# Kernel optimization log

Measured on AMD Instinct MI355X. Metric: run time of the kernel, lower is better.

Reference implementation:

```python
import jax, jax.numpy as jnp
import numpy as np

BLOCK = 32      # MX block size (elements sharing one scale)
EMAX = 8        # e4m3 max biased-unbias exponent (max normal = 448 = 2^8 * 1.75)
EMIN = -6       # e4m3 min normal exponent (values below handled as subnormal grid)
MAN_BITS = 3    # e4m3 mantissa bits
MAXVAL = 448.0  # e4m3 max representable magnitude


def _fp8_e4m3(x):
    """Round x to the nearest FP8 E4M3 representable value (saturating)."""
    absx = jnp.abs(x)
    # exponent of each element, clipped to normal range; EMIN clip gives the subnormal grid
    e = jnp.clip(jnp.floor(jnp.log2(jnp.where(absx > 0, absx, 1.0))), EMIN, EMAX)
    quantum = jnp.exp2(e - MAN_BITS)          # spacing of representable values at this exponent
    q = jnp.round(absx / quantum) * quantum   # round-to-nearest on that grid
    return jnp.sign(x) * jnp.minimum(q, MAXVAL)


def mx_fake_quant(x):
    """MX (microscaling) fake quantization: per-32-element power-of-two shared
    scale from block amax, elements stored as FP8 E4M3, then dequantized."""
    shape = x.shape
    xb = x.reshape(-1, BLOCK)                                   # [n_blocks, 32]
    amax = jnp.max(jnp.abs(xb), axis=-1, keepdims=True)         # [n_blocks, 1]
    # shared exponent: floor(log2(amax)) - emax_elem  (E8M0 power-of-two scale)
    shared_exp = jnp.floor(jnp.log2(jnp.where(amax > 0, amax, 1.0))) - EMAX
    scale = jnp.exp2(shared_exp)
    xq = _fp8_e4m3(xb / scale) * scale
    return xq.reshape(shape)


@jax.custom_vjp
def mx_ste(x):
    return mx_fake_quant(x)


def _mx_fwd(x):
    return mx_fake_quant(x), None


def _mx_bwd(_, g):
    return (g,)  # straight-through estimator


mx_ste.defvjp(_mx_fwd, _mx_bwd)


def setup_inputs() -> dict:
    key = jax.random.key(0)
    k1, k2 = jax.random.split(key)
    d_in, d_out = 256, 256
    x = jax.random.normal(k1, (16, 8192, d_in), dtype=jnp.float32)
    # lecun_normal init: std = 1/sqrt(fan_in)
    kernel = jax.random.normal(k2, (d_in, d_out), dtype=jnp.float32) * (1.0 / np.sqrt(d_in))
    bias = jnp.zeros((d_out,), dtype=jnp.float32)
    return {"x": x, "kernel": kernel, "bias": bias}


def reference(x, kernel, bias):
    xq = mx_ste(x)        # quantize_input=True
    kq = mx_ste(kernel)   # weight quantizer
    return jnp.dot(xq, kq) + bias
```

## Files before the change

### kernel.cpp

```cpp
#include <hip/hip_runtime.h>
#include <hip/hip_bf16.h>

typedef unsigned short u16;
typedef unsigned int u32;
typedef __attribute__((ext_vector_type(8))) short bf16x8;
typedef __attribute__((ext_vector_type(4))) float f32x4;
typedef __attribute__((ext_vector_type(2))) float f32x2;
typedef __attribute__((ext_vector_type(4))) unsigned short u16x4;

__device__ __forceinline__ void block_scale(float amax, float& scale, float& inv_scale) {
    int be = (int)(__float_as_uint(amax) >> 23);
    be = be < 8 ? 8 : be;
    scale     = __uint_as_float((unsigned)(be - 8) << 23);
    inv_scale = __uint_as_float((unsigned)(262 - be) << 23);
}

#if __has_builtin(__builtin_amdgcn_cvt_pk_fp8_f32) && __has_builtin(__builtin_amdgcn_cvt_pk_f32_fp8)
#define HAS_HW_FP8 1
#else
#define HAS_HW_FP8 0
#endif

#if !HAS_HW_FP8
__device__ __forceinline__ float mx_e4m3(float x, float inv_scale, float scale) {
    float v  = x * inv_scale;
    float av = fabsf(v);
    int e = (int)(__float_as_uint(av) >> 23) - 127;
    e = e < -6 ? -6 : (e > 8 ? 8 : e);
    float qs = __uint_as_float((unsigned)(130 - e) << 23);
    float qm = __uint_as_float((unsigned)(124 + e) << 23);
    float q  = fminf(rintf(av * qs) * qm, 448.0f);
    return copysignf(q, v) * scale;
}
#endif

__device__ __forceinline__ u16x4 quant4(float4 v, float inv, float sc) {
    u16x4 r;
#if HAS_HW_FP8
    float a = fminf(fmaxf(v.x * inv, -448.f), 448.f);
    float b = fminf(fmaxf(v.y * inv, -448.f), 448.f);
    float c = fminf(fmaxf(v.z * inv, -448.f), 448.f);
    float d = fminf(fmaxf(v.w * inv, -448.f), 448.f);
    int p = __builtin_amdgcn_cvt_pk_fp8_f32(a, b, 0, false);
    p     = __builtin_amdgcn_cvt_pk_fp8_f32(c, d, p, true);
    f32x2 lo = __builtin_amdgcn_cvt_pk_f32_fp8(p, false);
    f32x2 hi = __builtin_amdgcn_cvt_pk_f32_fp8(p, true);
    r.x = (u16)(__float_as_uint(lo[0] * sc) >> 16);
    r.y = (u16)(__float_as_uint(lo[1] * sc) >> 16);
    r.z = (u16)(__float_as_uint(hi[0] * sc) >> 16);
    r.w = (u16)(__float_as_uint(hi[1] * sc) >> 16);
#else
    r.x = (u16)(__float_as_uint(mx_e4m3(v.x, inv, sc)) >> 16);
    r.y = (u16)(__float_as_uint(mx_e4m3(v.y, inv, sc)) >> 16);
    r.z = (u16)(__float_as_uint(mx_e4m3(v.z, inv, sc)) >> 16);
    r.w = (u16)(__float_as_uint(mx_e4m3(v.w, inv, sc)) >> 16);
#endif
    return r;
}

__global__ void wq_kernel(const float* __restrict__ W, u16* __restrict__ Bq) {
    const int t  = blockIdx.x * blockDim.x + threadIdx.x;
    const int f  = t * 4;
    const int k  = f >> 8;
    const int n0 = f & 255;
    const float4 v = *(const float4*)(W + f);
    float am = fmaxf(fmaxf(fabsf(v.x), fabsf(v.y)), fmaxf(fabsf(v.z), fabsf(v.w)));
    am = fmaxf(am, __shfl_xor(am, 1));
    am = fmaxf(am, __shfl_xor(am, 2));
    am = fmaxf(am, __shfl_xor(am, 4));
    float sc, inv; block_scale(am, sc, inv);
    u16x4 q = quant4(v, inv, sc);
    Bq[(size_t)(n0 + 0) * 256 + k] = q.x;
    Bq[(size_t)(n0 + 1) * 256 + k] = q.y;
    Bq[(size_t)(n0 + 2) * 256 + k] = q.z;
    Bq[(size_t)(n0 + 3) * 256 + k] = q.w;
}

__global__ void __launch_bounds__(256, 4)
mx_gemm(const float* __restrict__ X, const u16* __restrict__ Bq,
        const float* __restrict__ bias, float* __restrict__ out)
{
    __shared__ u16 A[64 * 256];
    const int tid = threadIdx.x;
    const int w   = tid >> 6;
    const int l   = tid & 63;
    const size_t row0 = (size_t)blockIdx.x * 64;

    {
        const int kc = l * 4;
        float4 xv[16];
        #pragma unroll
        for (int it = 0; it < 16; ++it)
            xv[it] = *(const float4*)(X + (row0 + w * 16 + it) * 256 + kc);
        #pragma unroll
        for (int it = 0; it < 16; ++it) {
            const int r = w * 16 + it;
            float4 v = xv[it];
            float am = fmaxf(fmaxf(fabsf(v.x), fabsf(v.y)), fmaxf(fabsf(v.z), fabsf(v.w)));
            am = fmaxf(am, __shfl_xor(am, 1));
            am = fmaxf(am, __shfl_xor(am, 2));
            am = fmaxf(am, __shfl_xor(am, 4));
            float sc, inv; block_scale(am, sc, inv);
            u16x4 q = quant4(v, inv, sc);
            char* dst = (char*)A + (((u32)(r * 512 + l * 8)) ^ ((u32)(r & 7) << 4));
            *(u16x4*)dst = q;
        }
    }
    __syncthreads();

    const int lr = l & 15;
    const int lg = l >> 4;
    f32x4 acc[4][4] = {};
    const u16* bb = Bq + (size_t)(w * 64 + lr) * 256 + lg * 8;

    bf16x8 bcur[4], bnxt[4];
    #pragma unroll
    for (int ct = 0; ct < 4; ++ct)
        bcur[ct] = *(const bf16x8*)(bb + (size_t)ct * 16 * 256);

    #pragma unroll
    for (int ks = 0; ks < 8; ++ks) {
        bf16x8 af[4];
        #pragma unroll
        for (int rt = 0; rt < 4; ++rt) {
            const int row = rt * 16 + lr;
            const u32 off = ((u32)(row * 512 + ks * 64 + lg * 16)) ^ ((u32)(lr & 7) << 4);
            af[rt] = *(const bf16x8*)((const char*)A + off);
        }
        if (ks < 7) {
            #pragma unroll
            for (int ct = 0; ct < 4; ++ct)
                bnxt[ct] = *(const bf16x8*)(bb + (size_t)ct * 16 * 256 + (ks + 1) * 32);
        }
        #pragma unroll
        for (int rt = 0; rt < 4; ++rt)
            #pragma unroll
            for (int ct = 0; ct < 4; ++ct)
                acc[rt][ct] = __builtin_amdgcn_mfma_f32_16x16x32_bf16(
                    bcur[ct], af[rt], acc[rt][ct], 0, 0, 0);
        if (ks < 7) {
            #pragma unroll
            for (int ct = 0; ct < 4; ++ct) bcur[ct] = bnxt[ct];
        }
    }

    #pragma unroll
    for (int ct = 0; ct < 4; ++ct) {
        const float4 bv = *(const float4*)(bias + w * 64 + ct * 16 + lg * 4);
        #pragma unroll
        for (int rt = 0; rt < 4; ++rt) {
            f32x4 o = acc[rt][ct];
            o[0] += bv.x; o[1] += bv.y; o[2] += bv.z; o[3] += bv.w;
            *(f32x4*)(out + (row0 + rt * 16 + lr) * 256 + w * 64 + ct * 16 + lg * 4) = o;
        }
    }
}

extern "C" void kernel_launch(void* const* d_in, const int* in_sizes, int n_in,
                              void* d_out, int out_size, void* d_ws, size_t ws_size,
                              hipStream_t stream) {
    const float* x    = (const float*)d_in[0];
    const float* wk   = (const float*)d_in[1];
    const float* bias = (const float*)d_in[2];
    float* out = (float*)d_out;
    u16* Bq    = (u16*)d_ws;
    const int M = in_sizes[0] / 256;
    wq_kernel<<<64, 256, 0, stream>>>(wk, Bq);
    mx_gemm<<<M / 64, 256, 0, stream>>>(x, Bq, bias, out);
}
```

Before: 70.01 us.

## Load activations directly into MFMA register fragments, dropping the LDS staging

Each wavefront now owns 16 rows and all 256 output columns. It loads X straight into the MFMA A-fragment layout, quantizes in registers using a cross-lane amax shuffle over lanes 16 and 32, and skips the shared-memory tile and __syncthreads. The cost removed is the LDS write/read round trip and the block barrier. In exchange every wave streams the full 256x256 quantized weight matrix from global memory/L2, so B traffic per row rises 4x. The new layout also has uncoalesced strided X loads, and register pressure rises with launch_bounds min-blocks removed.

```diff
diff --git a/kernel.cpp b/kernel.cpp
--- a/kernel.cpp
+++ b/kernel.cpp
@@ -76,83 +76,63 @@
     Bq[(size_t)(n0 + 3) * 256 + k] = q.w;
 }
 
-__global__ void __launch_bounds__(256, 4)
+__global__ void __launch_bounds__(256)
 mx_gemm(const float* __restrict__ X, const u16* __restrict__ Bq,
         const float* __restrict__ bias, float* __restrict__ out)
 {
-    __shared__ u16 A[64 * 256];
     const int tid = threadIdx.x;
-    const int w   = tid >> 6;
     const int l   = tid & 63;
-    const size_t row0 = (size_t)blockIdx.x * 64;
+    const int lr  = l & 15;
+    const int lg  = l >> 4;
+    const size_t wv = (size_t)blockIdx.x * 4 + (tid >> 6);
+    const size_t r0 = wv * 16;
 
-    {
-        const int kc = l * 4;
-        float4 xv[16];
-        #pragma unroll
-        for (int it = 0; it < 16; ++it)
-            xv[it] = *(const float4*)(X + (row0 + w * 16 + it) * 256 + kc);
-        #pragma unroll
-        for (int it = 0; it < 16; ++it) {
-            const int r = w * 16 + it;
-            float4 v = xv[it];
-            float am = fmaxf(fmaxf(fabsf(v.x), fabsf(v.y)), fmaxf(fabsf(v.z), fabsf(v.w)));
-            am = fmaxf(am, __shfl_xor(am, 1));
-            am = fmaxf(am, __shfl_xor(am, 2));
-            am = fmaxf(am, __shfl_xor(am, 4));
-            float sc, inv; block_scale(am, sc, inv);
-            u16x4 q = quant4(v, inv, sc);
-            char* dst = (char*)A + (((u32)(r * 512 + l * 8)) ^ ((u32)(r & 7) << 4));
-            *(u16x4*)dst = q;
-        }
-    }
-    __syncthreads();
-
-    const int lr = l & 15;
-    const int lg = l >> 4;
-    f32x4 acc[4][4] = {};
-    const u16* bb = Bq + (size_t)(w * 64 + lr) * 256 + lg * 8;
-
-    bf16x8 bcur[4], bnxt[4];
-    #pragma unroll
-    for (int ct = 0; ct < 4; ++ct)
-        bcur[ct] = *(const bf16x8*)(bb + (size_t)ct * 16 * 256);
-
+    const float* xp = X + (r0 + lr) * 256 + lg * 8;
+    float4 xv[16];
     #pragma unroll
     for (int ks = 0; ks < 8; ++ks) {
-        bf16x8 af[4];
+        xv[2 * ks]     = *(const float4*)(xp + ks * 32);
+        xv[2 * ks + 1] = *(const float4*)(xp + ks * 32 + 4);
+    }
+
+    bf16x8 abf[8];
+    #pragma unroll
+    for (int ks = 0; ks < 8; ++ks) {
+        const float4 v0 = xv[2 * ks], v1 = xv[2 * ks + 1];
+        float am = fmaxf(fmaxf(fabsf(v0.x), fabsf(v0.y)), fmaxf(fabsf(v0.z), fabsf(v0.w)));
+        am = fmaxf(am, fmaxf(fmaxf(fabsf(v1.x), fabsf(v1.y)), fmaxf(fabsf(v1.z), fabsf(v1.w))));
+        am = fmaxf(am, __shfl_xor(am, 16));
+        am = fmaxf(am, __shfl_xor(am, 32));
+        float sc, inv; block_scale(am, sc, inv);
+        const u16x4 q0 = quant4(v0, inv, sc);
+        const u16x4 q1 = quant4(v1, inv, sc);
+        bf16x8 a;
+        a[0] = (short)q0.x; a[1] = (short)q0.y; a[2] = (short)q0.z; a[3] = (short)q0.w;
+        a[4] = (short)q1.x; a[5] = (short)q1.y; a[6] = (short)q1.z; a[7] = (short)q1.w;
+        abf[ks] = a;
+    }
+
+    f32x4 acc[16];
+    #pragma unroll
+    for (int ct = 0; ct < 16; ++ct) acc[ct] = (f32x4){0.f, 0.f, 0.f, 0.f};
+    const u16* bp = Bq + (size_t)lr * 256 + lg * 8;
+    #pragma unroll
+    for (int ct = 0; ct < 16; ++ct) {
+        const u16* bc = bp + (size_t)ct * 16 * 256;
         #pragma unroll
-        for (int rt = 0; rt < 4; ++rt) {
-            const int row = rt * 16 + lr;
-            const u32 off = ((u32)(row * 512 + ks * 64 + lg * 16)) ^ ((u32)(lr & 7) << 4);
-            af[rt] = *(const bf16x8*)((const char*)A + off);
-        }
-        if (ks < 7) {
-            #pragma unroll
-            for (int ct = 0; ct < 4; ++ct)
-                bnxt[ct] = *(const bf16x8*)(bb + (size_t)ct * 16 * 256 + (ks + 1) * 32);
-        }
-        #pragma unroll
-        for (int rt = 0; rt < 4; ++rt)
-            #pragma unroll
-            for (int ct = 0; ct < 4; ++ct)
-                acc[rt][ct] = __builtin_amdgcn_mfma_f32_16x16x32_bf16(
-                    bcur[ct], af[rt], acc[rt][ct], 0, 0, 0);
-        if (ks < 7) {
-            #pragma unroll
-            for (int ct = 0; ct < 4; ++ct) bcur[ct] = bnxt[ct];
+        for (int ks = 0; ks < 8; ++ks) {
+            const bf16x8 bf = *(const bf16x8*)(bc + ks * 32);
+            acc[ct] = __builtin_amdgcn_mfma_f32_16x16x32_bf16(bf, abf[ks], acc[ct], 0, 0, 0);
         }
     }
 
+    float* op = out + (r0 + lr) * 256 + lg * 4;
     #pragma unroll
-    for (int ct = 0; ct < 4; ++ct) {
-        const float4 bv = *(const float4*)(bias + w * 64 + ct * 16 + lg * 4);
-        #pragma unroll
-        for (int rt = 0; rt < 4; ++rt) {
-            f32x4 o = acc[rt][ct];
-            o[0] += bv.x; o[1] += bv.y; o[2] += bv.z; o[3] += bv.w;
-            *(f32x4*)(out + (row0 + rt * 16 + lr) * 256 + w * 64 + ct * 16 + lg * 4) = o;
-        }
+    for (int ct = 0; ct < 16; ++ct) {
+        const float4 bv = *(const float4*)(bias + ct * 16 + lg * 4);
+        f32x4 o = acc[ct];
+        o[0] += bv.x; o[1] += bv.y; o[2] += bv.z; o[3] += bv.w;
+        *(f32x4*)(op + ct * 16) = o;
     }
 }
 
```

New measurement: 179.2 us. 2.56x slower.

## Make GEMM blocks persistent over four row tiles with double-buffered quantized A

Applied to the files above, without the earlier changes.

Each workgroup now processes four 64-row tiles rather than one. The next tile's X values are prefetched into registers while the current tile runs its MFMAs, then quantized into a second LDS buffer after the output store. The aim is to overlap global X loads with compute and to amortize launch and bias loads. The cost is that LDS doubles to 64KB per block and launch bounds drop to 2 blocks per CU, which lowers occupancy and leaves fewer blocks (512) to spread across the CUs.

```diff
diff --git a/kernel.cpp b/kernel.cpp
--- a/kernel.cpp
+++ b/kernel.cpp
@@ -7,6 +7,8 @@
 typedef __attribute__((ext_vector_type(4))) float f32x4;
 typedef __attribute__((ext_vector_type(2))) float f32x2;
 typedef __attribute__((ext_vector_type(4))) unsigned short u16x4;
+
+#define T_TILES 4
 
 __device__ __forceinline__ void block_scale(float amax, float& scale, float& inv_scale) {
     int be = (int)(__float_as_uint(amax) >> 23);
@@ -76,83 +78,106 @@
     Bq[(size_t)(n0 + 3) * 256 + k] = q.w;
 }
 
-__global__ void __launch_bounds__(256, 4)
+__device__ __forceinline__ void quant_tile(const float4* xv, u16* Abuf,
+                                           int w, int l) {
+    #pragma unroll
+    for (int it = 0; it < 16; ++it) {
+        const int r = w * 16 + it;
+        float4 v = xv[it];
+        float am = fmaxf(fmaxf(fabsf(v.x), fabsf(v.y)), fmaxf(fabsf(v.z), fabsf(v.w)));
+        am = fmaxf(am, __shfl_xor(am, 1));
+        am = fmaxf(am, __shfl_xor(am, 2));
+        am = fmaxf(am, __shfl_xor(am, 4));
+        float sc, inv; block_scale(am, sc, inv);
+        u16x4 q = quant4(v, inv, sc);
+        char* dst = (char*)Abuf + (((u32)(r * 512 + l * 8)) ^ ((u32)(r & 7) << 4));
+        *(u16x4*)dst = q;
+    }
+}
+
+__global__ void __launch_bounds__(256, 2)
 mx_gemm(const float* __restrict__ X, const u16* __restrict__ Bq,
         const float* __restrict__ bias, float* __restrict__ out)
 {
-    __shared__ u16 A[64 * 256];
+    __shared__ u16 A[2][64 * 256];
     const int tid = threadIdx.x;
     const int w   = tid >> 6;
     const int l   = tid & 63;
-    const size_t row0 = (size_t)blockIdx.x * 64;
+    const int lr  = l & 15;
+    const int lg  = l >> 4;
+    const size_t row00 = (size_t)blockIdx.x * (64 * T_TILES);
 
-    {
-        const int kc = l * 4;
-        float4 xv[16];
-        #pragma unroll
-        for (int it = 0; it < 16; ++it)
-            xv[it] = *(const float4*)(X + (row0 + w * 16 + it) * 256 + kc);
-        #pragma unroll
-        for (int it = 0; it < 16; ++it) {
-            const int r = w * 16 + it;
-            float4 v = xv[it];
-            float am = fmaxf(fmaxf(fabsf(v.x), fabsf(v.y)), fmaxf(fabsf(v.z), fabsf(v.w)));
-            am = fmaxf(am, __shfl_xor(am, 1));
-            am = fmaxf(am, __shfl_xor(am, 2));
-            am = fmaxf(am, __shfl_xor(am, 4));
-            float sc, inv; block_scale(am, sc, inv);
-            u16x4 q = quant4(v, inv, sc);
-            char* dst = (char*)A + (((u32)(r * 512 + l * 8)) ^ ((u32)(r & 7) << 4));
-            *(u16x4*)dst = q;
-        }
-    }
+    const int kc = l * 4;
+    const float* xw = X + (row00 + w * 16) * 256 + kc;
+    float4 xv[16];
+
+    #pragma unroll
+    for (int it = 0; it < 16; ++it)
+        xv[it] = *(const float4*)(xw + it * 256);
+    __builtin_amdgcn_sched_barrier(0);
+    quant_tile(xv, &A[0][0], w, l);
     __syncthreads();
 
-    const int lr = l & 15;
-    const int lg = l >> 4;
-    f32x4 acc[4][4] = {};
     const u16* bb = Bq + (size_t)(w * 64 + lr) * 256 + lg * 8;
-
-    bf16x8 bcur[4], bnxt[4];
+    float4 bv[4];
     #pragma unroll
     for (int ct = 0; ct < 4; ++ct)
-        bcur[ct] = *(const bf16x8*)(bb + (size_t)ct * 16 * 256);
+        bv[ct] = *(const float4*)(bias + w * 64 + ct * 16 + lg * 4);
 
-    #pragma unroll
-    for (int ks = 0; ks < 8; ++ks) {
-        bf16x8 af[4];
+    for (int t = 0; t < T_TILES; ++t) {
+        if (t + 1 < T_TILES) {
+            const float* xn = xw + (size_t)(t + 1) * 64 * 256;
+            #pragma unroll
+            for (int it = 0; it < 16; ++it)
+                xv[it] = *(const float4*)(xn + it * 256);
+        }
+        __builtin_amdgcn_sched_barrier(0);
+
+        const u16* Ab = &A[t & 1][0];
+        f32x4 acc[4][4] = {};
+        bf16x8 bcur[4], bnxt[4];
         #pragma unroll
-        for (int rt = 0; rt < 4; ++rt) {
-            const int row = rt * 16 + lr;
-            const u32 off = ((u32)(row * 512 + ks * 64 + lg * 16)) ^ ((u32)(lr & 7) << 4);
-            af[rt] = *(const bf16x8*)((const char*)A + off);
+        for (int ct = 0; ct < 4; ++ct)
+            bcur[ct] = *(const bf16x8*)(bb + (size_t)ct * 16 * 256);
+        #pragma unroll
+        for (int ks = 0; ks < 8; ++ks) {
+            bf16x8 af[4];
+            #pragma unroll
+            for (int rt = 0; rt < 4; ++rt) {
+                const int row = rt * 16 + lr;
+                const u32 off = ((u32)(row * 512 + ks * 64 + lg * 16)) ^ ((u32)(lr & 7) << 4);
+                af[rt] = *(const bf16x8*)((const char*)Ab + off);
+            }
+            if (ks < 7) {
+                #pragma unroll
+                for (int ct = 0; ct < 4; ++ct)
+                    bnxt[ct] = *(const bf16x8*)(bb + (size_t)ct * 16 * 256 + (ks + 1) * 32);
+            }
+            #pragma unroll
+            for (int rt = 0; rt < 4; ++rt)
+                #pragma unroll
+                for (int ct = 0; ct < 4; ++ct)
+                    acc[rt][ct] = __builtin_amdgcn_mfma_f32_16x16x32_bf16(
+                        bcur[ct], af[rt], acc[rt][ct], 0, 0, 0);
+            if (ks < 7) {
+                #pragma unroll
+                for (int ct = 0; ct < 4; ++ct) bcur[ct] = bnxt[ct];
+            }
         }
-        if (ks < 7) {
+
+        const size_t row0 = row00 + (size_t)t * 64;
+        #pragma unroll
+        for (int ct = 0; ct < 4; ++ct)
             #pragma unroll
-            for (int ct = 0; ct < 4; ++ct)
-                bnxt[ct] = *(const bf16x8*)(bb + (size_t)ct * 16 * 256 + (ks + 1) * 32);
-        }
-        #pragma unroll
-        for (int rt = 0; rt < 4; ++rt)
-            #pragma unroll
-            for (int ct = 0; ct < 4; ++ct)
-                acc[rt][ct] = __builtin_amdgcn_mfma_f32_16x16x32_bf16(
-                    bcur[ct], af[rt], acc[rt][ct], 0, 0, 0);
-        if (ks < 7) {
-            #pragma unroll
-            for (int ct = 0; ct < 4; ++ct) bcur[ct] = bnxt[ct];
-        }
-    }
+            for (int rt = 0; rt < 4; ++rt) {
+                f32x4 o = acc[rt][ct];
+                o[0] += bv[ct].x; o[1] += bv[ct].y; o[2] += bv[ct].z; o[3] += bv[ct].w;
+                *(f32x4*)(out + (row0 + rt * 16 + lr) * 256 + w * 64 + ct * 16 + lg * 4) = o;
+            }
 
-    #pragma unroll
-    for (int ct = 0; ct < 4; ++ct) {
-        const float4 bv = *(const float4*)(bias + w * 64 + ct * 16 + lg * 4);
-        #pragma unroll
-        for (int rt = 0; rt < 4; ++rt) {
-            f32x4 o = acc[rt][ct];
-            o[0] += bv.x; o[1] += bv.y; o[2] += bv.z; o[3] += bv.w;
-            *(f32x4*)(out + (row0 + rt * 16 + lr) * 256 + w * 64 + ct * 16 + lg * 4) = o;
-        }
+        if (t + 1 < T_TILES)
+            quant_tile(xv, &A[(t + 1) & 1][0], w, l);
+        __syncthreads();
     }
 }
 
@@ -166,5 +191,5 @@
     u16* Bq    = (u16*)d_ws;
     const int M = in_sizes[0] / 256;
     wq_kernel<<<64, 256, 0, stream>>>(wk, Bq);
-    mx_gemm<<<M / 64, 256, 0, stream>>>(x, Bq, bias, out);
+    mx_gemm<<<M / (64 * T_TILES), 256, 0, stream>>>(x, Bq, bias, out);
 }
```

Result: slower. 134.1 us (+91.5%).
